# Kernel optimization log

Measured on AMD Instinct MI355X. Metric: run time of the kernel, lower is better.

Reference implementation:

```python
import jax, jax.numpy as jnp
import numpy as np

DIM = 768
HEADS = 12
HEAD_DIM = DIM // HEADS
EPS = 1e-5


def layernorm(x, gamma, beta):
    mu = jnp.mean(x, axis=-1, keepdims=True)
    var = jnp.var(x, axis=-1, keepdims=True)
    return (x - mu) * jax.lax.rsqrt(var + EPS) * gamma + beta


def setup_inputs() -> dict:
    key = jax.random.key(0)
    ks = jax.random.split(key, 9)
    B, N, C = 4, 2048, DIM
    s_in = 1.0 / np.sqrt(C)
    return {
        "x": jax.random.normal(ks[0], (B, N, C), dtype=jnp.float32),
        "qkv_w": jax.random.normal(ks[1], (3 * C, C), dtype=jnp.float32) * s_in,
        "qkv_b": jnp.zeros((3 * C,), dtype=jnp.float32),
        "proj_w": jax.random.normal(ks[2], (C, C), dtype=jnp.float32) * s_in,
        "proj_b": jnp.zeros((C,), dtype=jnp.float32),
        "q_gamma": jnp.ones((HEAD_DIM,), dtype=jnp.float32),
        "q_beta": jnp.zeros((HEAD_DIM,), dtype=jnp.float32),
        "k_gamma": jnp.ones((HEAD_DIM,), dtype=jnp.float32),
        "k_beta": jnp.zeros((HEAD_DIM,), dtype=jnp.float32),
    }


def reference(x, qkv_w, qkv_b, proj_w, proj_b, q_gamma, q_beta, k_gamma, k_beta):
    B, N, C = x.shape
    H, Dh = HEADS, C // HEADS
    scale = Dh ** (-0.5)
    # qkv projection: [B,N,3C] -> [3,B,H,N,Dh]
    qkv = (x @ qkv_w.T + qkv_b).reshape(B, N, 3, H, Dh).transpose(2, 0, 3, 1, 4)
    q, k, v = qkv[0], qkv[1], qkv[2]
    q = layernorm(q, q_gamma, q_beta)
    k = layernorm(k, k_gamma, k_beta)
    # explicit full score matrix [B,H,N,N] as in the original module
    attn = jnp.einsum("bhqd,bhkd->bhqk", q, k) * scale
    attn = jax.nn.softmax(attn, axis=-1)
    out = jnp.einsum("bhqk,bhkd->bhqd", attn, v)  # [B,H,N,Dh]
    out = out.transpose(0, 2, 1, 3).reshape(B, N, C)
    return out @ proj_w.T + proj_b
```

## Files before the change

kernel.cpp:

```cpp
#include <hip/hip_runtime.h>
#include <hip/hip_bf16.h>
#include <cstdint>
#include <cstddef>

#define BB 4
#define SEQ 2048
#define CD 768
#define NH 12
#define DH 64
#define MROWS (BB*SEQ)
#define NQKV (3*CD)

typedef float f32x4 __attribute__((ext_vector_type(4)));
typedef float f32x16 __attribute__((ext_vector_type(16)));
typedef short bf16x8 __attribute__((ext_vector_type(8)));

static __device__ __forceinline__ unsigned short f2bf(float f) {
  union { float f; unsigned int u; } cv; cv.f = f;
  unsigned int u = cv.u;
  unsigned int r = (u + 0x7FFFu + ((u >> 16) & 1u)) >> 16;
  return (unsigned short)r;
}

static __device__ __forceinline__ float fexp2(float x) {
#if __has_builtin(__builtin_amdgcn_exp2f)
  return __builtin_amdgcn_exp2f(x);
#else
  float r; asm("v_exp_f32 %0, %1" : "=v"(r) : "v"(x)); return r;
#endif
}

#define GAS __attribute__((address_space(1)))
#define LAS __attribute__((address_space(3)))
static __device__ __forceinline__ void gl2lds16(const void* g, void* l) {
  __builtin_amdgcn_global_load_lds((const GAS void*)g, (LAS void*)l, 16, 0, 0);
}

#define MFMA(a, b, c) __builtin_amdgcn_mfma_f32_16x16x32_bf16((a), (b), (c), 0, 0, 0)
#define MFMA32(a, b, c) __builtin_amdgcn_mfma_f32_32x32x16_bf16((a), (b), (c), 0, 0, 0)
#define PACKBF(dst, x, y) asm("v_cvt_pk_bf16_f32 %0, %1, %2" : "=v"(dst) : "v"(x), "v"(y))
#define SWAP32(a, b) asm("v_permlane32_swap_b32 %0, %1" : "+v"(a), "+v"(b))

#define QSC 0.18033688011112042f

#define CN1 (MROWS * CD / 4)
#define CN2 (CN1 + NQKV * CD / 4)
#define CN3 (CN2 + CD * CD / 4)
__global__ __launch_bounds__(256) void cvt_all(
    const float* __restrict__ x, const float* __restrict__ wq, const float* __restrict__ wp,
    unsigned short* __restrict__ Xb, unsigned short* __restrict__ Wq,
    unsigned short* __restrict__ Wp) {
  int i = blockIdx.x * 256 + threadIdx.x;
  if (i >= CN3) return;
  const float* src;
  unsigned short* dst;
  int k;
  if (i < CN1) { src = x; dst = Xb; k = i; }
  else if (i < CN2) { src = wq; dst = Wq; k = i - CN1; }
  else { src = wp; dst = Wp; k = i - CN2; }
  float4 v = reinterpret_cast<const float4*>(src)[k];
  unsigned int lo = (unsigned int)f2bf(v.x) | ((unsigned int)f2bf(v.y) << 16);
  unsigned int hi = (unsigned int)f2bf(v.z) | ((unsigned int)f2bf(v.w) << 16);
  reinterpret_cast<uint2*>(dst)[k] = make_uint2(lo, hi);
}

__global__ __launch_bounds__(256) void qkv_gemm(
    const unsigned short* __restrict__ Xb, const unsigned short* __restrict__ Wb,
    const float* __restrict__ bias,
    const float* __restrict__ qg, const float* __restrict__ qbt,
    const float* __restrict__ kg, const float* __restrict__ kbt,
    unsigned short* __restrict__ Qo, unsigned short* __restrict__ Ko,
    unsigned short* __restrict__ Vt) {
  __shared__ unsigned short smem[4 * 128 * 64];
#define ALS(buf) (&smem[(buf) * 8192])
#define BLS(buf) (&smem[16384 + (buf) * 8192])
  const int tid = threadIdx.x;
  const int wid = tid >> 6, lane = tid & 63;
  const int g = lane >> 4, cl = lane & 15;
  const int wr = (wid >> 1) * 64, wc = (wid & 1) * 64;

  const int wg = blockIdx.x;
  const int wgid = (wg & 7) * 144 + (wg >> 3);
  const int bm = wgid / 18, bn = wgid % 18;

  f32x4 acc[4][4] = {};

  const int srow = tid >> 3;
  const int scol = ((tid & 7) ^ (srow & 7)) * 8;
  const unsigned short* Abase = Xb + (size_t)(bm * 128 + srow) * CD + scol;
  const unsigned short* Bbase = Wb + (size_t)(bn * 128 + srow) * CD + scol;

#define QSTG(buf, kt)                                                         \
  do {                                                                        \
    gl2lds16(Abase + (size_t)0 * 32 * CD + (kt) * 64, ALS(buf) + 0 * 2048 + tid * 8); \
    gl2lds16(Abase + (size_t)1 * 32 * CD + (kt) * 64, ALS(buf) + 1 * 2048 + tid * 8); \
    gl2lds16(Abase + (size_t)2 * 32 * CD + (kt) * 64, ALS(buf) + 2 * 2048 + tid * 8); \
    gl2lds16(Abase + (size_t)3 * 32 * CD + (kt) * 64, ALS(buf) + 3 * 2048 + tid * 8); \
    gl2lds16(Bbase + (size_t)0 * 32 * CD + (kt) * 64, BLS(buf) + 0 * 2048 + tid * 8); \
    gl2lds16(Bbase + (size_t)1 * 32 * CD + (kt) * 64, BLS(buf) + 1 * 2048 + tid * 8); \
    gl2lds16(Bbase + (size_t)2 * 32 * CD + (kt) * 64, BLS(buf) + 2 * 2048 + tid * 8); \
    gl2lds16(Bbase + (size_t)3 * 32 * CD + (kt) * 64, BLS(buf) + 3 * 2048 + tid * 8); \
  } while (0)

  QSTG(0, 0);
  __syncthreads();
  const int NKT = CD / 64;
  for (int kt = 0; kt < NKT; ++kt) {
    const int cur = kt & 1;
    if (kt + 1 < NKT) QSTG(cur ^ 1, kt + 1);
    bf16x8 bfr[4][2];
#pragma unroll
    for (int j = 0; j < 4; ++j) {
      const int Bcol = wc + j * 16 + cl;
      const int sw = (Bcol & 7) << 3;
      bfr[j][0] = *(const bf16x8*)&BLS(cur)[Bcol * 64 + ((g * 8) ^ sw)];
      bfr[j][1] = *(const bf16x8*)&BLS(cur)[Bcol * 64 + ((32 + g * 8) ^ sw)];
    }
    __builtin_amdgcn_s_setprio(1);
#pragma unroll
    for (int i = 0; i < 4; ++i) {
      const int Arow = wr + i * 16 + cl;
      const int sw = (Arow & 7) << 3;
      bf16x8 a0 = *(const bf16x8*)&ALS(cur)[Arow * 64 + ((g * 8) ^ sw)];
      bf16x8 a1 = *(const bf16x8*)&ALS(cur)[Arow * 64 + ((32 + g * 8) ^ sw)];
#pragma unroll
      for (int j = 0; j < 4; ++j) {
        acc[i][j] = MFMA(a0, bfr[j][0], acc[i][j]);
        acc[i][j] = MFMA(a1, bfr[j][1], acc[i][j]);
      }
    }
    __builtin_amdgcn_s_setprio(0);
    __syncthreads();
  }
#undef QSTG

  float* cb = (float*)smem;
#define CIDX(r, c) ((r) * 128 + (((((c) >> 2)) ^ ((r) & 31)) << 2) + ((c) & 3))
#pragma unroll
  for (int i = 0; i < 4; ++i)
#pragma unroll
    for (int j = 0; j < 4; ++j)
#pragma unroll
      for (int r = 0; r < 4; ++r)
        cb[CIDX(wr + i * 16 + g * 4 + r, wc + j * 16 + cl)] = acc[i][j][r];
  __syncthreads();

  const int t = bn / 6;
  const int h0 = (bn % 6) * 2;
  const int j0 = bn * 128;

  if (t == 2) {
    const int col = tid >> 1, nh = tid & 1;
    const int h = h0 + (col >> 6), d = col & 63;
    const float bia = bias[j0 + col];
    const int m0 = bm * 128;
    const int b = m0 >> 11;
    const int nn0 = (m0 & 2047) + nh * 64;
    unsigned short* dst = &Vt[((size_t)(b * NH + h) * DH + d) * SEQ + nn0];
#pragma unroll
    for (int k8 = 0; k8 < 8; ++k8) {
      union { unsigned short us[8]; uint4 v; } u;
#pragma unroll
      for (int e = 0; e < 8; ++e)
        u.us[e] = f2bf(cb[CIDX(nh * 64 + k8 * 8 + e, col)] + bia);
      *reinterpret_cast<uint4*>(&dst[k8 * 8]) = u.v;
    }
    return;
  }

  const int nl = tid >> 1, half = tid & 1;
  const int h = h0 + half;
  const int m = bm * 128 + nl;
  const int b = m >> 11, n = m & 2047;
  const float* gmp = (t == 0) ? qg : kg;
  const float* btp = (t == 0) ? qbt : kbt;
  const float sc = (t == 0) ? QSC : 1.0f;
  const float* bi = bias + j0 + half * 64;

  float v[64];
#pragma unroll
  for (int k4 = 0; k4 < 16; ++k4) {
    f32x4 q = *(const f32x4*)&cb[nl * 128 + ((((half * 16 + k4)) ^ (nl & 31)) << 2)];
    float4 b4 = reinterpret_cast<const float4*>(bi)[k4];
    v[k4 * 4 + 0] = q[0] + b4.x;
    v[k4 * 4 + 1] = q[1] + b4.y;
    v[k4 * 4 + 2] = q[2] + b4.z;
    v[k4 * 4 + 3] = q[3] + b4.w;
  }
  float s0 = 0, s1 = 0, s2 = 0, s3 = 0, q0 = 0, q1 = 0, q2 = 0, q3 = 0;
#pragma unroll
  for (int k = 0; k < 64; k += 4) {
    s0 += v[k]; q0 += v[k] * v[k];
    s1 += v[k + 1]; q1 += v[k + 1] * v[k + 1];
    s2 += v[k + 2]; q2 += v[k + 2] * v[k + 2];
    s3 += v[k + 3]; q3 += v[k + 3] * v[k + 3];
  }
  const float sum = (s0 + s1) + (s2 + s3);
  const float ssum = (q0 + q1) + (q2 + q3);
  const float mu = sum * (1.0f / 64.0f);
  const float var = ssum * (1.0f / 64.0f) - mu * mu;
  const float rstd = rsqrtf(var + 1e-5f);

  unsigned short* dst = ((t == 0) ? Qo : Ko) + ((size_t)(b * NH + h) * SEQ + n) * DH;
#pragma unroll
  for (int k8 = 0; k8 < 8; ++k8) {
    float4 gm4 = reinterpret_cast<const float4*>(gmp)[k8 * 2];
    float4 gm4b = reinterpret_cast<const float4*>(gmp)[k8 * 2 + 1];
    float4 bt4 = reinterpret_cast<const float4*>(btp)[k8 * 2];
    float4 bt4b = reinterpret_cast<const float4*>(btp)[k8 * 2 + 1];
    const float* g8 = &gm4.x;
    const float* b8 = &bt4.x;
    union { unsigned short us[8]; uint4 vv; } u;
#pragma unroll
    for (int e = 0; e < 4; ++e) {
      u.us[e] = f2bf(((v[k8 * 8 + e] - mu) * rstd * (&gm4.x)[e] + (&bt4.x)[e]) * sc);
      u.us[4 + e] = f2bf(((v[k8 * 8 + 4 + e] - mu) * rstd * (&gm4b.x)[e] + (&bt4b.x)[e]) * sc);
    }
    (void)g8; (void)b8;
    *reinterpret_cast<uint4*>(&dst[k8 * 8]) = u.vv;
  }
#undef CIDX
#undef ALS
#undef BLS
}

__global__ __launch_bounds__(256, 3) void attn_fwd(
    const unsigned short* __restrict__ Qb, const unsigned short* __restrict__ Kb,
    const unsigned short* __restrict__ Vtb, unsigned short* __restrict__ Ob) {
  __shared__ unsigned short kl[2][64 * 64];
  __shared__ unsigned short vt[2][64 * 64];
  __shared__ float linv[4][32];
  const int tid = threadIdx.x, wave = tid >> 6, lane = tid & 63;
  const int q32 = lane & 31, hi = lane >> 5;

  const int wg = blockIdx.x;
  const int lin = (wg & 7) * 96 + (wg >> 3);
  const int bh = lin >> 4;
  const int qbase = (lin & 15) * 128 + wave * 32;

  const unsigned short* qrow = Qb + ((size_t)bh * SEQ + qbase + q32) * DH + hi * 8;
  bf16x8 qf[4];
#pragma unroll
  for (int dc = 0; dc < 4; ++dc) qf[dc] = *(const bf16x8*)&qrow[dc * 16];

  const unsigned short* Kh = Kb + (size_t)bh * SEQ * DH;
  const unsigned short* Vth = Vtb + (size_t)bh * DH * SEQ;

  const int sr = tid >> 3;
  const int sc = 8 * ((tid & 7) ^ (sr & 7));
  const int ksw = (q32 & 7) << 3;

#define ASTAGE(buf, kb0)                                                      \
  do {                                                                        \
    gl2lds16(&Kh[(size_t)((kb0) + sr) * DH + sc], &kl[buf][tid * 8]);         \
    gl2lds16(&Kh[(size_t)((kb0) + sr + 32) * DH + sc], &kl[buf][tid * 8 + 2048]); \
    gl2lds16(&Vth[(size_t)sr * SEQ + (kb0) + sc], &vt[buf][tid * 8]);         \
    gl2lds16(&Vth[(size_t)(sr + 32) * SEQ + (kb0) + sc], &vt[buf][tid * 8 + 2048]); \
  } while (0)

  f32x16 o0 = {}, o1 = {};
  float su0 = 0.0f, su1 = 0.0f, su2 = 0.0f, su3 = 0.0f;

  ASTAGE(0, 0);
  __syncthreads();
  const int NT = SEQ / 64;
#pragma unroll 2
  for (int it = 0; it < NT; ++it) {
    const int cur = it & 1;
    if (it + 1 < NT) ASTAGE(cur ^ 1, (it + 1) * 64);

    f32x16 s0 = {}, s1 = {};
    __builtin_amdgcn_s_setprio(1);
#pragma unroll
    for (int dc = 0; dc < 4; ++dc) {
      const int colb = dc * 16 + hi * 8;
      bf16x8 kf0 = *(const bf16x8*)&kl[cur][q32 * 64 + (colb ^ ksw)];
      bf16x8 kf1 = *(const bf16x8*)&kl[cur][(32 + q32) * 64 + (colb ^ ksw)];
      s0 = MFMA32(kf0, qf[dc], s0);
      s1 = MFMA32(kf1, qf[dc], s1);
    }
    __builtin_amdgcn_s_setprio(0);

#pragma unroll
    for (int r = 0; r < 16; r += 4) {
      s0[r + 0] = fexp2(s0[r + 0]); su0 += s0[r + 0];
      s0[r + 1] = fexp2(s0[r + 1]); su1 += s0[r + 1];
      s0[r + 2] = fexp2(s0[r + 2]); su2 += s0[r + 2];
      s0[r + 3] = fexp2(s0[r + 3]); su3 += s0[r + 3];
    }
#pragma unroll
    for (int r = 0; r < 16; r += 4) {
      s1[r + 0] = fexp2(s1[r + 0]); su0 += s1[r + 0];
      s1[r + 1] = fexp2(s1[r + 1]); su1 += s1[r + 1];
      s1[r + 2] = fexp2(s1[r + 2]); su2 += s1[r + 2];
      s1[r + 3] = fexp2(s1[r + 3]); su3 += s1[r + 3];
    }

    bf16x8 pav[4];
#pragma unroll
    for (int c = 0; c < 4; ++c) {
      const int b = 8 * (c & 1);
      unsigned int wA0, wA1, wB0, wB1;
      if (c < 2) {
        PACKBF(wA0, s0[b + 0], s0[b + 1]); PACKBF(wA1, s0[b + 2], s0[b + 3]);
        PACKBF(wB0, s0[b + 4], s0[b + 5]); PACKBF(wB1, s0[b + 6], s0[b + 7]);
      } else {
        PACKBF(wA0, s1[b + 0], s1[b + 1]); PACKBF(wA1, s1[b + 2], s1[b + 3]);
        PACKBF(wB0, s1[b + 4], s1[b + 5]); PACKBF(wB1, s1[b + 6], s1[b + 7]);
      }
      SWAP32(wA0, wB0);
      SWAP32(wA1, wB1);
      union { unsigned int w[4]; bf16x8 v; } u;
      u.w[0] = wA0; u.w[1] = wA1; u.w[2] = wB0; u.w[3] = wB1;
      pav[c] = u.v;
    }

    __builtin_amdgcn_s_setprio(1);
#pragma unroll
    for (int c = 0; c < 4; ++c) {
      const int colb = c * 16 + hi * 8;
      bf16x8 vf0 = *(const bf16x8*)&vt[cur][q32 * 64 + (colb ^ ksw)];
      bf16x8 vf1 = *(const bf16x8*)&vt[cur][(32 + q32) * 64 + (colb ^ ksw)];
      o0 = MFMA32(pav[c], vf0, o0);
      o1 = MFMA32(pav[c], vf1, o1);
    }
    __builtin_amdgcn_s_setprio(0);
    __syncthreads();
  }
#undef ASTAGE

  float lsum = (su0 + su1) + (su2 + su3);
  lsum += __shfl_xor(lsum, 32, 64);
  linv[wave][q32] = __builtin_amdgcn_rcpf(lsum);
  __syncthreads();

  const int b = bh / NH, h = bh % NH;
#pragma unroll
  for (int r = 0; r < 16; ++r) {
    const int qq = (r & 3) + 8 * (r >> 2) + 4 * hi;
    const float iv = linv[wave][qq];
    size_t base = ((size_t)(b * SEQ + qbase + qq)) * CD + h * DH;
    Ob[base + q32] = f2bf(o0[r] * iv);
    Ob[base + 32 + q32] = f2bf(o1[r] * iv);
  }
}

__global__ __launch_bounds__(256) void proj_gemm(
    const unsigned short* __restrict__ Ab, const unsigned short* __restrict__ Wb,
    const float* __restrict__ bias, float* __restrict__ out) {
  __shared__ unsigned short Als[2][128 * 64];
  __shared__ unsigned short Bls[2][128 * 64];
  const int tid = threadIdx.x;
  const int wid = tid >> 6, lane = tid & 63;
  const int g = lane >> 4, cl = lane & 15;
  const int bm = blockIdx.x, bn = blockIdx.y;
  const int wr = (wid >> 1) * 64, wc = (wid & 1) * 64;

  f32x4 acc[4][4] = {};

  const int srow = tid >> 3;
  const int scol = ((tid & 7) ^ (srow & 7)) * 8;
  const unsigned short* Abase = Ab + (size_t)(bm * 128 + srow) * CD + scol;
  const unsigned short* Bbase = Wb + (size_t)(bn * 128 + srow) * CD + scol;

#define PSTG(buf, kt)                                                         \
  do {                                                                        \
    gl2lds16(Abase + (size_t)0 * 32 * CD + (kt) * 64, &Als[buf][0 * 2048 + tid * 8]); \
    gl2lds16(Abase + (size_t)1 * 32 * CD + (kt) * 64, &Als[buf][1 * 2048 + tid * 8]); \
    gl2lds16(Abase + (size_t)2 * 32 * CD + (kt) * 64, &Als[buf][2 * 2048 + tid * 8]); \
    gl2lds16(Abase + (size_t)3 * 32 * CD + (kt) * 64, &Als[buf][3 * 2048 + tid * 8]); \
    gl2lds16(Bbase + (size_t)0 * 32 * CD + (kt) * 64, &Bls[buf][0 * 2048 + tid * 8]); \
    gl2lds16(Bbase + (size_t)1 * 32 * CD + (kt) * 64, &Bls[buf][1 * 2048 + tid * 8]); \
    gl2lds16(Bbase + (size_t)2 * 32 * CD + (kt) * 64, &Bls[buf][2 * 2048 + tid * 8]); \
    gl2lds16(Bbase + (size_t)3 * 32 * CD + (kt) * 64, &Bls[buf][3 * 2048 + tid * 8]); \
  } while (0)

  PSTG(0, 0);
  __syncthreads();
  const int NKT = CD / 64;
  for (int kt = 0; kt < NKT; ++kt) {
    const int cur = kt & 1;
    if (kt + 1 < NKT) PSTG(cur ^ 1, kt + 1);
    bf16x8 bfr[4][2];
#pragma unroll
    for (int j = 0; j < 4; ++j) {
      const int Bcol = wc + j * 16 + cl;
      const int sw = (Bcol & 7) << 3;
      bfr[j][0] = *(const bf16x8*)&Bls[cur][Bcol * 64 + ((g * 8) ^ sw)];
      bfr[j][1] = *(const bf16x8*)&Bls[cur][Bcol * 64 + ((32 + g * 8) ^ sw)];
    }
    __builtin_amdgcn_s_setprio(1);
#pragma unroll
    for (int i = 0; i < 4; ++i) {
      const int Arow = wr + i * 16 + cl;
      const int sw = (Arow & 7) << 3;
      bf16x8 a0 = *(const bf16x8*)&Als[cur][Arow * 64 + ((g * 8) ^ sw)];
      bf16x8 a1 = *(const bf16x8*)&Als[cur][Arow * 64 + ((32 + g * 8) ^ sw)];
#pragma unroll
      for (int j = 0; j < 4; ++j) {
        acc[i][j] = MFMA(a0, bfr[j][0], acc[i][j]);
        acc[i][j] = MFMA(a1, bfr[j][1], acc[i][j]);
      }
    }
    __builtin_amdgcn_s_setprio(0);
    __syncthreads();
  }
#undef PSTG

  const int j0 = bn * 128 + wc;
  float pb4[4];
#pragma unroll
  for (int j = 0; j < 4; ++j) pb4[j] = bias[j0 + j * 16 + cl];
#pragma unroll
  for (int i = 0; i < 4; ++i) {
#pragma unroll
    for (int r = 0; r < 4; ++r) {
      const int m = bm * 128 + wr + i * 16 + g * 4 + r;
      float* orow = out + (size_t)m * CD + j0;
#pragma unroll
      for (int j = 0; j < 4; ++j) orow[j * 16 + cl] = acc[i][j][r] + pb4[j];
    }
  }
}

extern "C" void kernel_launch(void* const* d_in, const int* in_sizes, int n_in,
                              void* d_out, int out_size, void* d_ws, size_t ws_size,
                              hipStream_t stream) {
  const float* x = (const float*)d_in[0];
  const float* qkv_w = (const float*)d_in[1];
  const float* qkv_b = (const float*)d_in[2];
  const float* proj_w = (const float*)d_in[3];
  const float* proj_b = (const float*)d_in[4];
  const float* q_gamma = (const float*)d_in[5];
  const float* q_beta = (const float*)d_in[6];
  const float* k_gamma = (const float*)d_in[7];
  const float* k_beta = (const float*)d_in[8];
  float* out = (float*)d_out;

  char* w = (char*)d_ws;
  unsigned short* Xb = (unsigned short*)w; w += (size_t)MROWS * CD * 2;
  unsigned short* Wq = (unsigned short*)w; w += (size_t)NQKV * CD * 2;
  unsigned short* Wp = (unsigned short*)w; w += (size_t)CD * CD * 2;
  unsigned short* Qo = (unsigned short*)w; w += (size_t)BB * NH * SEQ * DH * 2;
  unsigned short* Ko = (unsigned short*)w; w += (size_t)BB * NH * SEQ * DH * 2;
  unsigned short* Vt = (unsigned short*)w; w += (size_t)BB * NH * SEQ * DH * 2;
  unsigned short* Ob = (unsigned short*)w; w += (size_t)MROWS * CD * 2;

  cvt_all<<<(CN3 + 255) / 256, 256, 0, stream>>>(x, qkv_w, proj_w, Xb, Wq, Wp);

  qkv_gemm<<<(MROWS / 128) * (NQKV / 128), 256, 0, stream>>>(
      Xb, Wq, qkv_b, q_gamma, q_beta, k_gamma, k_beta, Qo, Ko, Vt);

  attn_fwd<<<SEQ / 128 * BB * NH, 256, 0, stream>>>(Qo, Ko, Vt, Ob);

  proj_gemm<<<dim3(MROWS / 128, CD / 128), 256, 0, stream>>>(Ob, Wp, proj_b, out);
}
```

Before: 133.8 us.

## Software-pipeline attention loop with triple-buffered K/V and overlapped QK compute

The attention loop now triple-buffers the K and V^T tiles in shared memory. It computes the QK scores of the next tile before running softmax and the PV product on the current tile, with the loop unrolled by two over alternating score registers. The goal is to let the score MFMAs for one tile overlap the exp/pack VALU work and PV MFMAs of the previous one, and to prefetch K/V two tiles ahead. In exchange, shared memory per block grows by half and a second set of score accumulators raises register pressure, which could cause spills under the 3-blocks-per-CU launch bound. A small cleanup also removes unused pointers in the layernorm kernel.

```diff
diff --git a/kernel.cpp b/kernel.cpp
--- a/kernel.cpp
+++ b/kernel.cpp
@@ -208,15 +208,12 @@
     float4 gm4b = reinterpret_cast<const float4*>(gmp)[k8 * 2 + 1];
     float4 bt4 = reinterpret_cast<const float4*>(btp)[k8 * 2];
     float4 bt4b = reinterpret_cast<const float4*>(btp)[k8 * 2 + 1];
-    const float* g8 = &gm4.x;
-    const float* b8 = &bt4.x;
     union { unsigned short us[8]; uint4 vv; } u;
 #pragma unroll
     for (int e = 0; e < 4; ++e) {
       u.us[e] = f2bf(((v[k8 * 8 + e] - mu) * rstd * (&gm4.x)[e] + (&bt4.x)[e]) * sc);
       u.us[4 + e] = f2bf(((v[k8 * 8 + 4 + e] - mu) * rstd * (&gm4b.x)[e] + (&bt4b.x)[e]) * sc);
     }
-    (void)g8; (void)b8;
     *reinterpret_cast<uint4*>(&dst[k8 * 8]) = u.vv;
   }
 #undef CIDX
@@ -227,8 +224,8 @@
 __global__ __launch_bounds__(256, 3) void attn_fwd(
     const unsigned short* __restrict__ Qb, const unsigned short* __restrict__ Kb,
     const unsigned short* __restrict__ Vtb, unsigned short* __restrict__ Ob) {
-  __shared__ unsigned short kl[2][64 * 64];
-  __shared__ unsigned short vt[2][64 * 64];
+  __shared__ unsigned short kl[3][64 * 64];
+  __shared__ unsigned short vt[3][64 * 64];
   __shared__ float linv[4][32];
   const int tid = threadIdx.x, wave = tid >> 6, lane = tid & 63;
   const int q32 = lane & 31, hi = lane >> 5;
@@ -258,76 +255,94 @@
     gl2lds16(&Vth[(size_t)(sr + 32) * SEQ + (kb0) + sc], &vt[buf][tid * 8 + 2048]); \
   } while (0)
 
+#define QKCOMP(bufc, S0, S1)                                                  \
+  do {                                                                        \
+    S0 = (f32x16){};                                                          \
+    S1 = (f32x16){};                                                          \
+    __builtin_amdgcn_s_setprio(1);                                            \
+    _Pragma("unroll")                                                         \
+    for (int dc = 0; dc < 4; ++dc) {                                          \
+      const int colb = dc * 16 + hi * 8;                                      \
+      bf16x8 kf0 = *(const bf16x8*)&kl[bufc][q32 * 64 + (colb ^ ksw)];        \
+      bf16x8 kf1 = *(const bf16x8*)&kl[bufc][(32 + q32) * 64 + (colb ^ ksw)]; \
+      S0 = MFMA32(kf0, qf[dc], S0);                                           \
+      S1 = MFMA32(kf1, qf[dc], S1);                                           \
+    }                                                                         \
+    __builtin_amdgcn_s_setprio(0);                                            \
+  } while (0)
+
+#define SOFTPV(S0, S1, bufv)                                                  \
+  do {                                                                        \
+    _Pragma("unroll")                                                         \
+    for (int r = 0; r < 16; r += 4) {                                         \
+      S0[r + 0] = fexp2(S0[r + 0]); su0 += S0[r + 0];                         \
+      S0[r + 1] = fexp2(S0[r + 1]); su1 += S0[r + 1];                         \
+      S0[r + 2] = fexp2(S0[r + 2]); su2 += S0[r + 2];                         \
+      S0[r + 3] = fexp2(S0[r + 3]); su3 += S0[r + 3];                         \
+    }                                                                         \
+    _Pragma("unroll")                                                         \
+    for (int r = 0; r < 16; r += 4) {                                         \
+      S1[r + 0] = fexp2(S1[r + 0]); su0 += S1[r + 0];                         \
+      S1[r + 1] = fexp2(S1[r + 1]); su1 += S1[r + 1];                         \
+      S1[r + 2] = fexp2(S1[r + 2]); su2 += S1[r + 2];                         \
+      S1[r + 3] = fexp2(S1[r + 3]); su3 += S1[r + 3];                         \
+    }                                                                         \
+    bf16x8 pav[4];                                                            \
+    _Pragma("unroll")                                                         \
+    for (int c = 0; c < 4; ++c) {                                             \
+      const int b = 8 * (c & 1);                                              \
+      unsigned int wA0, wA1, wB0, wB1;                                        \
+      if (c < 2) {                                                            \
+        PACKBF(wA0, S0[b + 0], S0[b + 1]); PACKBF(wA1, S0[b + 2], S0[b + 3]); \
+        PACKBF(wB0, S0[b + 4], S0[b + 5]); PACKBF(wB1, S0[b + 6], S0[b + 7]); \
+      } else {                                                                \
+        PACKBF(wA0, S1[b + 0], S1[b + 1]); PACKBF(wA1, S1[b + 2], S1[b + 3]); \
+        PACKBF(wB0, S1[b + 4], S1[b + 5]); PACKBF(wB1, S1[b + 6], S1[b + 7]); \
+      }                                                                       \
+      SWAP32(wA0, wB0);                                                       \
+      SWAP32(wA1, wB1);                                                       \
+      union { unsigned int w[4]; bf16x8 v; } u;                               \
+      u.w[0] = wA0; u.w[1] = wA1; u.w[2] = wB0; u.w[3] = wB1;                 \
+      pav[c] = u.v;                                                           \
+    }                                                                         \
+    __builtin_amdgcn_s_setprio(1);                                            \
+    _Pragma("unroll")                                                         \
+    for (int c = 0; c < 4; ++c) {                                             \
+      const int colb = c * 16 + hi * 8;                                       \
+      bf16x8 vf0 = *(const bf16x8*)&vt[bufv][q32 * 64 + (colb ^ ksw)];        \
+      bf16x8 vf1 = *(const bf16x8*)&vt[bufv][(32 + q32) * 64 + (colb ^ ksw)]; \
+      o0 = MFMA32(pav[c], vf0, o0);                                           \
+      o1 = MFMA32(pav[c], vf1, o1);                                           \
+    }                                                                         \
+    __builtin_amdgcn_s_setprio(0);                                            \
+  } while (0)
+
   f32x16 o0 = {}, o1 = {};
+  f32x16 sa0, sa1, sb0, sb1;
   float su0 = 0.0f, su1 = 0.0f, su2 = 0.0f, su3 = 0.0f;
 
+  const int NT = SEQ / 64;
   ASTAGE(0, 0);
+  ASTAGE(1, 64);
   __syncthreads();
-  const int NT = SEQ / 64;
-#pragma unroll 2
-  for (int it = 0; it < NT; ++it) {
-    const int cur = it & 1;
-    if (it + 1 < NT) ASTAGE(cur ^ 1, (it + 1) * 64);
-
-    f32x16 s0 = {}, s1 = {};
-    __builtin_amdgcn_s_setprio(1);
-#pragma unroll
-    for (int dc = 0; dc < 4; ++dc) {
-      const int colb = dc * 16 + hi * 8;
-      bf16x8 kf0 = *(const bf16x8*)&kl[cur][q32 * 64 + (colb ^ ksw)];
-      bf16x8 kf1 = *(const bf16x8*)&kl[cur][(32 + q32) * 64 + (colb ^ ksw)];
-      s0 = MFMA32(kf0, qf[dc], s0);
-      s1 = MFMA32(kf1, qf[dc], s1);
-    }
-    __builtin_amdgcn_s_setprio(0);
-
-#pragma unroll
-    for (int r = 0; r < 16; r += 4) {
-      s0[r + 0] = fexp2(s0[r + 0]); su0 += s0[r + 0];
-      s0[r + 1] = fexp2(s0[r + 1]); su1 += s0[r + 1];
-      s0[r + 2] = fexp2(s0[r + 2]); su2 += s0[r + 2];
-      s0[r + 3] = fexp2(s0[r + 3]); su3 += s0[r + 3];
-    }
-#pragma unroll
-    for (int r = 0; r < 16; r += 4) {
-      s1[r + 0] = fexp2(s1[r + 0]); su0 += s1[r + 0];
-      s1[r + 1] = fexp2(s1[r + 1]); su1 += s1[r + 1];
-      s1[r + 2] = fexp2(s1[r + 2]); su2 += s1[r + 2];
-      s1[r + 3] = fexp2(s1[r + 3]); su3 += s1[r + 3];
-    }
-
-    bf16x8 pav[4];
-#pragma unroll
-    for (int c = 0; c < 4; ++c) {
-      const int b = 8 * (c & 1);
-      unsigned int wA0, wA1, wB0, wB1;
-      if (c < 2) {
-        PACKBF(wA0, s0[b + 0], s0[b + 1]); PACKBF(wA1, s0[b + 2], s0[b + 3]);
-        PACKBF(wB0, s0[b + 4], s0[b + 5]); PACKBF(wB1, s0[b + 6], s0[b + 7]);
-      } else {
-        PACKBF(wA0, s1[b + 0], s1[b + 1]); PACKBF(wA1, s1[b + 2], s1[b + 3]);
-        PACKBF(wB0, s1[b + 4], s1[b + 5]); PACKBF(wB1, s1[b + 6], s1[b + 7]);
-      }
-      SWAP32(wA0, wB0);
-      SWAP32(wA1, wB1);
-      union { unsigned int w[4]; bf16x8 v; } u;
-      u.w[0] = wA0; u.w[1] = wA1; u.w[2] = wB0; u.w[3] = wB1;
-      pav[c] = u.v;
-    }
-
-    __builtin_amdgcn_s_setprio(1);
-#pragma unroll
-    for (int c = 0; c < 4; ++c) {
-      const int colb = c * 16 + hi * 8;
-      bf16x8 vf0 = *(const bf16x8*)&vt[cur][q32 * 64 + (colb ^ ksw)];
-      bf16x8 vf1 = *(const bf16x8*)&vt[cur][(32 + q32) * 64 + (colb ^ ksw)];
-      o0 = MFMA32(pav[c], vf0, o0);
-      o1 = MFMA32(pav[c], vf1, o1);
-    }
-    __builtin_amdgcn_s_setprio(0);
+  QKCOMP(0, sa0, sa1);
+
+  for (int t = 0; t + 2 < NT; t += 2) {
+    ASTAGE((t + 2) % 3, (t + 2) * 64);
+    QKCOMP((t + 1) % 3, sb0, sb1);
+    SOFTPV(sa0, sa1, t % 3);
     __syncthreads();
-  }
+    if (t + 3 < NT) ASTAGE((t + 3) % 3, (t + 3) * 64);
+    QKCOMP((t + 2) % 3, sa0, sa1);
+    SOFTPV(sb0, sb1, (t + 1) % 3);
+    __syncthreads();
+  }
+  QKCOMP((NT - 1) % 3, sb0, sb1);
+  SOFTPV(sa0, sa1, (NT - 2) % 3);
+  SOFTPV(sb0, sb1, (NT - 1) % 3);
 #undef ASTAGE
+#undef QKCOMP
+#undef SOFTPV
 
   float lsum = (su0 + su1) + (su2 + su3);
   lsum += __shfl_xor(lsum, 32, 64);
```

Result: slower. 204.7 us (+53.0%).
